# Performance work log

Hardware: AMD Instinct MI355X
Metric: run time of the kernel (lower is better)

Reference implementation:

```python
import jax, jax.numpy as jnp
import numpy as np
import math

S, HID = 2048, 2048
NH, Q_LORA, KV_LORA = 16, 1536, 512
NOPE, ROPE, VDIM = 128, 64, 128
HEAD = NOPE + ROPE  # 192
BLK = 128
EPS = 1e-6
MSCALE = 0.1 * 1.0 * math.log(40.0) + 1.0
SOFTMAX_SCALE = HEAD ** -0.5 * MSCALE * MSCALE


def _dequant(w, s, blk=BLK):
    # w: [out,in] stored quantized values, s: [ceil(out/blk), ceil(in/blk)] block scale_inv
    so = jnp.repeat(s, blk, axis=0)[: w.shape[0]]
    se = jnp.repeat(so, blk, axis=1)[:, : w.shape[1]]
    return w * se


def _mm_dq(x, w, s):
    # mm_w8a16_dq_forward: x @ dequant(w).T
    return x @ _dequant(w, s).T


def _rmsnorm(x, w, eps=EPS):
    var = jnp.mean(x * x, axis=-1, keepdims=True)
    return x * jax.lax.rsqrt(var + eps) * w


def _rotate_half(x):
    h = x.shape[-1] // 2
    return jnp.concatenate([-x[..., h:], x[..., :h]], axis=-1)


def setup_inputs() -> dict:
    key = jax.random.key(0)
    ks = jax.random.split(key, 16)
    d = {
        'hidden_states': jax.random.normal(ks[0], (S, HID), jnp.float32),
        'wq_a': jax.random.normal(ks[1], (Q_LORA, HID), jnp.float32),
        'sq_a': jax.random.uniform(ks[2], (12, 16), jnp.float32) * 0.02 + 0.005,
        'wq_b': jax.random.normal(ks[3], (NH * HEAD, Q_LORA), jnp.float32),
        'sq_b': jax.random.uniform(ks[4], (24, 12), jnp.float32) * 0.02 + 0.005,
        'wkv_a': jax.random.normal(ks[5], (KV_LORA + ROPE, HID), jnp.float32),
        'skv_a': jax.random.uniform(ks[6], (5, 16), jnp.float32) * 0.02 + 0.005,
        'wkv_b': jax.random.normal(ks[7], (NH * (NOPE + VDIM), KV_LORA), jnp.float32),
        'skv_b': jax.random.uniform(ks[8], (32, 4), jnp.float32) * 0.02 + 0.005,
        'wo': jax.random.normal(ks[9], (HID, NH * VDIM), jnp.float32),
        'so': jax.random.uniform(ks[10], (16, 16), jnp.float32) * 0.02 + 0.005,
        'q_ln_w': jnp.ones((Q_LORA,), jnp.float32),
        'kv_ln_w': jnp.ones((KV_LORA,), jnp.float32),
    }
    pos = jnp.arange(S, dtype=jnp.float32)[:, None]
    inv = 1.0 / (10000.0 ** (jnp.arange(0, ROPE, 2, dtype=jnp.float32) / ROPE))
    ang = pos * inv[None, :]
    ang = jnp.concatenate([ang, ang], axis=-1)  # [S, 64]
    d['cos'] = jnp.cos(ang)
    d['sin'] = jnp.sin(ang)
    return d


def reference(hidden_states, cos, sin, wq_a, sq_a, wq_b, sq_b, wkv_a, skv_a,
              wkv_b, skv_b, wo, so, q_ln_w, kv_ln_w):
    # Q low-rank path: q_a -> rmsnorm -> q_b
    lq = _mm_dq(hidden_states, wq_a, sq_a)                 # [S, q_lora]
    q = _mm_dq(_rmsnorm(lq, q_ln_w), wq_b, sq_b)           # [S, NH*HEAD]
    q = q.reshape(S, NH, HEAD)
    q_nope, q_pe = q[..., :NOPE], q[..., NOPE:]            # [S,NH,128], [S,NH,64]

    # KV low-rank + MQA rope path
    lkv = _mm_dq(hidden_states, wkv_a, skv_a)              # [S, kv_lora+rope]
    kv_nope = _rmsnorm(lkv[:, :KV_LORA], kv_ln_w)          # [S, kv_lora]
    k_pe = lkv[:, KV_LORA:]                                # [S, 64] (shared across heads)
    kvb = _mm_dq(kv_nope, wkv_b, skv_b).reshape(S, NH, NOPE + VDIM)
    k_nope, v = kvb[..., :NOPE], kvb[..., NOPE:]           # [S,NH,128] each

    # RoPE (rotate-half) on the pe parts
    q_pe = q_pe * cos[:, None, :] + _rotate_half(q_pe) * sin[:, None, :]
    k_pe = k_pe * cos + _rotate_half(k_pe) * sin           # [S, 64]

    # prefill MLA attention with causal mask
    scores = (jnp.einsum('shd,thd->hst', q_nope, k_nope)
              + jnp.einsum('shd,td->hst', q_pe, k_pe)) * SOFTMAX_SCALE
    causal = jnp.tril(jnp.ones((S, S), bool))
    scores = jnp.where(causal[None], scores, -jnp.inf)
    probs = jax.nn.softmax(scores, axis=-1)                # [NH,S,S]
    attn = jnp.einsum('hst,thd->shd', probs, v).reshape(S, NH * VDIM)

    return _mm_dq(attn, wo, so)                            # [S, HID]
```

## Files before the change

### kernel.cpp

```cpp
#include <hip/hip_runtime.h>

typedef unsigned short u16;
typedef unsigned int u32;
typedef __attribute__((ext_vector_type(8))) short bf16x8;
typedef __attribute__((ext_vector_type(4))) float f32x4;
typedef __attribute__((ext_vector_type(16))) float f32x16;
typedef __attribute__((ext_vector_type(4))) unsigned short u16x4;

#define S_LEN 2048
#define HIDDEN 2048
#define NHEAD 16
#define QLORA 1536
#define KVLORA 512
#define NOPE_D 128
#define ROPE_D 64
#define V_D 128
#define HEAD_D 192
#define NCOMB 2176
#define LOG2E 1.442695041f

__device__ __constant__ float SM_SCALE_C = (float)(0.07216878364870323 *
    ((0.1 * 3.6888794541139363 + 1.0) * (0.1 * 3.6888794541139363 + 1.0)));

__device__ inline u16 f2bf(float f) {
    union { float f; unsigned int u; } v; v.f = f;
    unsigned int r = v.u + 0x7FFFu + ((v.u >> 16) & 1u);
    return (u16)(r >> 16);
}
__device__ inline float bf2f(u16 b) {
    union { unsigned int u; float f; } v; v.u = ((unsigned int)b) << 16;
    return v.f;
}
__device__ inline void gload_lds16(const u16* g, u16* l) {
    __builtin_amdgcn_global_load_lds(
        (const __attribute__((address_space(1))) void*)g,
        (__attribute__((address_space(3))) void*)l, 16, 0, 0);
}
__device__ __forceinline__ void dequant_row8(const float* __restrict__ W, const float* __restrict__ Sc,
                                             u16* __restrict__ out, int n, int K, int sc_cols, int k) {
    float sc = Sc ? Sc[(n >> 7) * sc_cols + (k >> 7)] : 1.0f;
    f32x4 v0 = *(const f32x4*)(W + (size_t)n * K + k);
    f32x4 v1 = *(const f32x4*)(W + (size_t)n * K + k + 4);
    bf16x8 o;
    #pragma unroll
    for (int i = 0; i < 4; ++i) {
        o[i]     = (short)f2bf(v0[i] * sc);
        o[i + 4] = (short)f2bf(v1[i] * sc);
    }
    *(bf16x8*)(out + (size_t)n * K + k) = o;
}

__device__ __forceinline__ int xcd_swizzle(int orig, int nwg) {
    int qq = nwg >> 3, rr = nwg & 7, xcd = orig & 7, loc = orig >> 3;
    return (xcd < rr) ? (xcd * (qq + 1) + loc)
                      : (rr * (qq + 1) + (xcd - rr) * qq + loc);
}

__device__ __forceinline__ void gemm_core(
    const u16* __restrict__ A, const u16* __restrict__ W, u16* __restrict__ C,
    int M, int N, int Ktot, int Ksub, int bm, int bn, int bz,
    u16* As, u16* Ws) {
    const int tid = threadIdx.x;
    const int lane = tid & 63;
    const int wv = tid >> 6;
    const int wm = wv >> 1, wn = wv & 1;
    const int lr = lane & 15, lk = lane >> 4;
    const int srow = lane >> 3;
    const int schunk = lane & 7;

    f32x4 acc[4][4] = {};

    const int kbeg = bz * Ksub;
    const int kend = kbeg + Ksub;
    for (int k0 = kbeg; k0 < kend; k0 += 64) {
        __syncthreads();
        #pragma unroll
        for (int i = 0; i < 4; ++i) {
            int t = (wv * 4 + i) * 8 + srow;
            int cs = (schunk ^ (t & 7)) << 3;
            gload_lds16(A + (size_t)(bm + t) * Ktot + k0 + cs, &As[(wv * 4 + i) * 512]);
            gload_lds16(W + (size_t)(bn + t) * Ktot + k0 + cs, &Ws[(wv * 4 + i) * 512]);
        }
        __syncthreads();
        #pragma unroll
        for (int kh = 0; kh < 2; ++kh) {
            bf16x8 af[4], bfr[4];
            #pragma unroll
            for (int mi = 0; mi < 4; ++mi) {
                int r = wm * 64 + mi * 16 + lr;
                af[mi] = *(const bf16x8*)&As[r * 64 + (((kh * 4 + lk) ^ (lr & 7)) << 3)];
            }
            #pragma unroll
            for (int ni = 0; ni < 4; ++ni) {
                int r = wn * 64 + ni * 16 + lr;
                bfr[ni] = *(const bf16x8*)&Ws[r * 64 + (((kh * 4 + lk) ^ (lr & 7)) << 3)];
            }
            #pragma unroll
            for (int mi = 0; mi < 4; ++mi)
                #pragma unroll
                for (int ni = 0; ni < 4; ++ni)
                    acc[mi][ni] = __builtin_amdgcn_mfma_f32_16x16x32_bf16(af[mi], bfr[ni], acc[mi][ni], 0, 0, 0);
        }
    }

    u16* Pb = C + (size_t)bz * M * N;
    #pragma unroll
    for (int mi = 0; mi < 4; ++mi)
        #pragma unroll
        for (int ni = 0; ni < 4; ++ni)
            #pragma unroll
            for (int j = 0; j < 4; ++j) {
                int r = bm + wm * 64 + mi * 16 + lk * 4 + j;
                int c = bn + wn * 64 + ni * 16 + lr;
                if (c < N) Pb[(size_t)r * N + c] = f2bf(acc[mi][ni][j]);
            }
}

__global__ __launch_bounds__(256)
void prep_weights_a(const float* __restrict__ hs,
                    const float* __restrict__ wq_a, const float* __restrict__ sq_a,
                    const float* __restrict__ wkv_a, const float* __restrict__ skv_a,
                    u16* __restrict__ hs_bf, u16* __restrict__ wcomb) {
    int r = blockIdx.x * 4 + (threadIdx.x >> 6);
    const float* W; const float* Sc; u16* out; int n, sc_cols;
    if (r < 2048)      { W = hs;    Sc = 0;      out = hs_bf; n = r;        sc_cols = 0; }
    else if (r < 3584) { W = wq_a;  Sc = sq_a;   out = wcomb; n = r - 2048; sc_cols = 16; }
    else               { W = wkv_a; Sc = skv_a;  out = wcomb + (size_t)QLORA * 2048; n = r - 3584; sc_cols = 16; }
    for (int k = (threadIdx.x & 63) * 8; k < 2048; k += 512)
        dequant_row8(W, Sc, out, n, 2048, sc_cols, k);
}

__global__ __launch_bounds__(256)
void gemm_comb_prepw(const u16* __restrict__ hs_bf, const u16* __restrict__ wcomb,
                     u16* __restrict__ arena,
                     const float* __restrict__ wq_b, const float* __restrict__ sq_b,
                     const float* __restrict__ wkv_b, const float* __restrict__ skv_b,
                     const float* __restrict__ wo, const float* __restrict__ so,
                     u16* __restrict__ wqb_bf, u16* __restrict__ wkvb_bf,
                     u16* __restrict__ wo_bf) {
    __shared__ u16 As[128 * 64];
    __shared__ u16 Ws[128 * 64];
    const int NWG = 17 * 16 * 4 + 2304;
    const int wg = xcd_swizzle(blockIdx.x, NWG);
    if (wg < 17 * 16 * 4) {
        const int bn = (wg % 17) * 128;
        const int bm = ((wg / 17) % 16) * 128;
        const int bz = wg / (17 * 16);
        gemm_core(hs_bf, wcomb, arena, S_LEN, NCOMB, HIDDEN, HIDDEN / 4, bm, bn, bz, As, Ws);
    } else {
        const int w2 = wg - 17 * 16 * 4;
        int r = w2 * 4 + (threadIdx.x >> 6);
        const float* W; const float* Sc; u16* out; int n, K, sc_cols;
        if (r < 3072)      { W = wq_b;  Sc = sq_b;  out = wqb_bf;  n = r;        K = 1536; sc_cols = 12; }
        else if (r < 7168) { W = wkv_b; Sc = skv_b; out = wkvb_bf; n = r - 3072; K = 512;  sc_cols = 4; }
        else               { W = wo;    Sc = so;    out = wo_bf;   n = r - 7168; K = 2048; sc_cols = 16; }
        for (int k = (threadIdx.x & 63) * 8; k < K; k += 512)
            dequant_row8(W, Sc, out, n, K, sc_cols, k);
    }
}

__global__ __launch_bounds__(256)
void gemm_bf16(const u16* __restrict__ A, const u16* __restrict__ W,
               u16* __restrict__ C, int M, int N, int Ktot, int Ksub) {
    __shared__ u16 As[128 * 64];
    __shared__ u16 Ws[128 * 64];
    const int gx = gridDim.x, gy = gridDim.y;
    const int nwg = gx * gy * gridDim.z;
    const int orig = blockIdx.x + gx * (blockIdx.y + gy * blockIdx.z);
    const int wg = xcd_swizzle(orig, nwg);
    const int bn = (wg % gx) * 128;
    const int bm = ((wg / gx) % gy) * 128;
    const int bz = wg / (gx * gy);
    gemm_core(A, W, C, M, N, Ktot, Ksub, bm, bn, bz, As, Ws);
}

__global__ __launch_bounds__(256)
void gemm_qh_kvb(const u16* __restrict__ lqn, const u16* __restrict__ wqb, u16* __restrict__ arena,
                 const u16* __restrict__ kvn, const u16* __restrict__ wkvb, u16* __restrict__ kvb) {
    __shared__ u16 As[128 * 64];
    __shared__ u16 Ws[128 * 64];
    const int NWG = 24 * 16 * 3 + 32 * 16;
    const int wg = xcd_swizzle(blockIdx.x, NWG);
    if (wg < 24 * 16 * 3) {
        const int bn = (wg % 24) * 128;
        const int bm = ((wg / 24) % 16) * 128;
        const int bz = wg / (24 * 16);
        gemm_core(lqn, wqb, arena, S_LEN, NHEAD * HEAD_D, QLORA, 512, bm, bn, bz, As, Ws);
    } else {
        const int w2 = wg - 24 * 16 * 3;
        const int bn = (w2 % 32) * 128;
        const int bm = (w2 / 32) * 128;
        gemm_core(kvn, wkvb, kvb, S_LEN, NHEAD * 256, KVLORA, 512, bm, bn, 0, As, Ws);
    }
}

__global__ __launch_bounds__(256)
void reduce_rms_comb(const u16* __restrict__ P,
                     const float* __restrict__ q_ln, const float* __restrict__ kv_ln,
                     u16* __restrict__ lqn, u16* __restrict__ kvn, u16* __restrict__ kpe) {
    __shared__ float vbuf[NCOMB];
    __shared__ float r2[2][4];
    const int row = blockIdx.x;
    const u16* p0 = P + (size_t)row * NCOMB;
    const size_t st = (size_t)S_LEN * NCOMB;
    float ssq = 0.f, ssk = 0.f;
    for (int c = threadIdx.x * 8; c < NCOMB; c += 2048) {
        bf16x8 a0 = *(const bf16x8*)(p0 + c);
        bf16x8 a1 = *(const bf16x8*)(p0 + st + c);
        bf16x8 a2 = *(const bf16x8*)(p0 + 2 * st + c);
        bf16x8 a3 = *(const bf16x8*)(p0 + 3 * st + c);
        float s = 0.f;
        #pragma unroll
        for (int j = 0; j < 8; ++j) {
            float v = bf2f((u16)a0[j]) + bf2f((u16)a1[j]) + bf2f((u16)a2[j]) + bf2f((u16)a3[j]);
            vbuf[c + j] = v;
            s += v * v;
        }
        if (c < QLORA) ssq += s;
        else if (c < QLORA + KVLORA) ssk += s;
    }
    #pragma unroll
    for (int off = 1; off < 64; off <<= 1) {
        ssq += __shfl_xor(ssq, off, 64);
        ssk += __shfl_xor(ssk, off, 64);
    }
    if ((threadIdx.x & 63) == 0) {
        r2[0][threadIdx.x >> 6] = ssq;
        r2[1][threadIdx.x >> 6] = ssk;
    }
    __syncthreads();
    float rsq = rsqrtf((r2[0][0] + r2[0][1] + r2[0][2] + r2[0][3]) / (float)QLORA + 1e-6f);
    float rsk = rsqrtf((r2[1][0] + r2[1][1] + r2[1][2] + r2[1][3]) / (float)KVLORA + 1e-6f);
    for (int c = threadIdx.x * 8; c < NCOMB; c += 2048) {
        bf16x8 o;
        if (c < QLORA) {
            #pragma unroll
            for (int j = 0; j < 8; ++j) o[j] = (short)f2bf(vbuf[c + j] * rsq * q_ln[c + j]);
            *(bf16x8*)(lqn + (size_t)row * QLORA + c) = o;
        } else if (c < QLORA + KVLORA) {
            int cc = c - QLORA;
            #pragma unroll
            for (int j = 0; j < 8; ++j) o[j] = (short)f2bf(vbuf[c + j] * rsk * kv_ln[cc + j]);
            *(bf16x8*)(kvn + (size_t)row * KVLORA + cc) = o;
        } else if (c < QLORA + KVLORA + ROPE_D) {
            int cc = c - QLORA - KVLORA;
            #pragma unroll
            for (int j = 0; j < 8; ++j) o[j] = (short)f2bf(vbuf[c + j]);
            *(bf16x8*)(kpe + (size_t)row * ROPE_D + cc) = o;
        }
    }
}

__global__ __launch_bounds__(256)
void prep_qkv_frag(const u16* __restrict__ P, const u16* __restrict__ kvb,
                   const u16* __restrict__ kpe, const float* __restrict__ cosb,
                   const float* __restrict__ sinb, u16* __restrict__ qfrag,
                   u16* __restrict__ kfrag, u16* __restrict__ vfrag) {
    __shared__ u16 Vs[32][136];
    const int sblk = blockIdx.x, h = blockIdx.y;
    if (blockIdx.z == 0) {
        const float sm = SM_SCALE_C;
        const size_t st = (size_t)S_LEN * (NHEAD * HEAD_D);
        #pragma unroll
        for (int c = 0; c < 3; ++c) {
            int idx = c * 256 + threadIdx.x;
            int kk = idx >> 6;
            int lane = idx & 63;
            int s = sblk * 32 + (lane & 31);
            int d0 = kk * 16 + (lane >> 5) * 8;
            const u16* p0 = P + (size_t)s * (NHEAD * HEAD_D) + h * HEAD_D;
            float x[8];
            {
                bf16x8 a0 = *(const bf16x8*)(p0 + d0);
                bf16x8 a1 = *(const bf16x8*)(p0 + st + d0);
                bf16x8 a2 = *(const bf16x8*)(p0 + 2 * st + d0);
                #pragma unroll
                for (int j = 0; j < 8; ++j)
                    x[j] = bf2f((u16)a0[j]) + bf2f((u16)a1[j]) + bf2f((u16)a2[j]);
            }
            bf16x8 o;
            if (d0 < NOPE_D) {
                #pragma unroll
                for (int j = 0; j < 8; ++j) o[j] = (short)f2bf(x[j] * sm);
            } else {
                int r0 = d0 - NOPE_D;
                int rp = (r0 + 32) & 63;
                float rv[8];
                bf16x8 b0 = *(const bf16x8*)(p0 + NOPE_D + rp);
                bf16x8 b1 = *(const bf16x8*)(p0 + st + NOPE_D + rp);
                bf16x8 b2 = *(const bf16x8*)(p0 + 2 * st + NOPE_D + rp);
                #pragma unroll
                for (int j = 0; j < 8; ++j)
                    rv[j] = bf2f((u16)b0[j]) + bf2f((u16)b1[j]) + bf2f((u16)b2[j]);
                float sign = (r0 < 32) ? -1.f : 1.f;
                #pragma unroll
                for (int j = 0; j < 8; ++j) {
                    float cs = cosb[s * ROPE_D + r0 + j];
                    float sn = sinb[s * ROPE_D + r0 + j];
                    o[j] = (short)f2bf((x[j] * cs + sign * rv[j] * sn) * sm);
                }
            }
            *(bf16x8*)(qfrag + (((size_t)h * 64 + sblk) * 12 + kk) * 512 + lane * 8) = o;
        }
    } else {
        #pragma unroll
        for (int it = 0; it < 2; ++it) {
            int idx = it * 256 + threadIdx.x;
            int r = idx >> 4;
            int c8 = (idx & 15) * 8;
            int s = sblk * 32 + r;
            *(bf16x8*)&Vs[r][c8] = *(const bf16x8*)(kvb + (size_t)s * (NHEAD * 256) + h * 256 + NOPE_D + c8);
        }
        #pragma unroll
        for (int c = 0; c < 3; ++c) {
            int idx = c * 256 + threadIdx.x;
            int kk = idx >> 6;
            int lane = idx & 63;
            int s = sblk * 32 + (lane & 31);
            int d0 = kk * 16 + (lane >> 5) * 8;
            bf16x8 o;
            if (d0 < NOPE_D) {
                o = *(const bf16x8*)(kvb + (size_t)s * (NHEAD * 256) + h * 256 + d0);
            } else {
                int r0 = d0 - NOPE_D;
                const u16* kp = kpe + (size_t)s * ROPE_D;
                bf16x8 x = *(const bf16x8*)(kp + r0);
                bf16x8 rv = *(const bf16x8*)(kp + ((r0 + 32) & 63));
                float sign = (r0 < 32) ? -1.f : 1.f;
                #pragma unroll
                for (int j = 0; j < 8; ++j) {
                    float cs = cosb[s * ROPE_D + r0 + j];
                    float sn = sinb[s * ROPE_D + r0 + j];
                    o[j] = (short)f2bf(bf2f((u16)x[j]) * cs + sign * bf2f((u16)rv[j]) * sn);
                }
            }
            *(bf16x8*)(kfrag + (((size_t)h * 64 + sblk) * 12 + kk) * 512 + lane * 8) = o;
        }
        __syncthreads();
        #pragma unroll
        for (int it = 0; it < 2; ++it) {
            int idx = it * 256 + threadIdx.x;
            int fi = idx >> 6;
            int lane = idx & 63;
            int bb = fi >> 1, h16 = fi & 1;
            int col = bb * 32 + (lane & 31);
            int row0 = h16 * 16 + (lane >> 5) * 8;
            bf16x8 o;
            #pragma unroll
            for (int j = 0; j < 8; ++j) o[j] = (short)Vs[row0 + j][col];
            *(bf16x8*)(vfrag + (((size_t)h * 64 + sblk) * 8 + fi) * 512 + lane * 8) = o;
        }
    }
}

__global__ void reduce_out(const u16* __restrict__ P, float* __restrict__ out, int n) {
    int i = (blockIdx.x * blockDim.x + threadIdx.x) * 8;
    if (i >= n) return;
    bf16x8 a0 = *(const bf16x8*)(P + i);
    bf16x8 a1 = *(const bf16x8*)(P + (size_t)n + i);
    bf16x8 a2 = *(const bf16x8*)(P + 2 * (size_t)n + i);
    bf16x8 a3 = *(const bf16x8*)(P + 3 * (size_t)n + i);
    f32x4 o0, o1;
    #pragma unroll
    for (int j = 0; j < 4; ++j) {
        o0[j] = bf2f((u16)a0[j]) + bf2f((u16)a1[j]) + bf2f((u16)a2[j]) + bf2f((u16)a3[j]);
        o1[j] = bf2f((u16)a0[j + 4]) + bf2f((u16)a1[j + 4]) + bf2f((u16)a2[j + 4]) + bf2f((u16)a3[j + 4]);
    }
    *(f32x4*)(out + i) = o0;
    *(f32x4*)(out + i + 4) = o1;
}

__global__ __launch_bounds__(256, 2)
void flash_attn4(const u16* __restrict__ qfrag, const u16* __restrict__ kfrag,
                 const u16* __restrict__ vfrag, u16* __restrict__ attn) {
    __shared__ float OB[3][128][32];
    __shared__ float MB[3][2][32];

    const int tid = threadIdx.x, lane = tid & 63, wq = tid >> 6;
    const int b = blockIdx.x;
    const int t = 63 - (b >> 4);
    const int h = ((b & 7) << 1) | ((b >> 3) & 1);
    const int q0 = t * 32;
    const int lq = lane & 31;
    const int hi = lane >> 5;

    const int n = t + 1;
    const int s_lo = (wq * n) >> 2;
    const int s_hi = ((wq + 1) * n) >> 2;

    bf16x8 qfr[12];
    {
        const u16* qb = qfrag + (((size_t)h * 64 + t) * 12) * 512 + lane * 8;
        #pragma unroll
        for (int kk = 0; kk < 12; ++kk) qfr[kk] = *(const bf16x8*)(qb + kk * 512);
    }

    const u16* kfb = kfrag + ((size_t)h * 64 * 12) * 512 + lane * 8;
    const u16* vfb = vfrag + ((size_t)h * 64 * 8) * 512 + lane * 8;

    f32x16 oa[4] = {};
    float mrun = -3.0e38f, lrun = 0.f;

    bf16x8 kcur[12];
    {
        int psub = (s_lo < s_hi) ? s_lo : 0;
        const u16* kp = kfb + (size_t)psub * 12 * 512;
        #pragma unroll
        for (int kk = 0; kk < 12; ++kk)
            kcur[kk] = *(const bf16x8*)(kp + kk * 512);
    }

    for (int sub = s_lo; sub < s_hi; ++sub) {
        f32x16 s0 = {}, s1 = {};
        __builtin_amdgcn_s_setprio(1);
        #pragma unroll
        for (int kk = 0; kk < 12; kk += 2) {
            s0 = __builtin_amdgcn_mfma_f32_32x32x16_bf16(kcur[kk], qfr[kk], s0, 0, 0, 0);
            s1 = __builtin_amdgcn_mfma_f32_32x32x16_bf16(kcur[kk + 1], qfr[kk + 1], s1, 0, 0, 0);
        }
        __builtin_amdgcn_s_setprio(0);
        {
            int nsub = (sub + 1 < s_hi) ? sub + 1 : sub;
            const u16* kp = kfb + (size_t)nsub * 12 * 512;
            #pragma unroll
            for (int kk = 0; kk < 12; ++kk)
                kcur[kk] = *(const bf16x8*)(kp + kk * 512);
        }
        bf16x8 va[8];
        {
            const u16* vp = vfb + (size_t)sub * 8 * 512;
            #pragma unroll
            for (int fi = 0; fi < 8; ++fi)
                va[fi] = *(const bf16x8*)(vp + fi * 512);
        }
        f32x16 sv = s0 + s1;
        if (sub == t) {
            #pragma unroll
            for (int r = 0; r < 16; ++r) {
                int krow = (r & 3) + 8 * (r >> 2) + 4 * hi;
                if (krow > lq) sv[r] = -3.0e38f;
            }
        }
        float tm = sv[0];
        #pragma unroll
        for (int r = 1; r < 16; ++r) tm = fmaxf(tm, sv[r]);
        tm = fmaxf(tm, __shfl_xor(tm, 32, 64));
        if (!__all(tm - mrun <= 8.f)) {
            float mn = fmaxf(mrun, tm);
            float scl = exp2f((mrun - mn) * LOG2E);
            mrun = mn;
            lrun *= scl;
            #pragma unroll
            for (int bb = 0; bb < 4; ++bb)
                #pragma unroll
                for (int r = 0; r < 16; ++r) oa[bb][r] *= scl;
        }
        float p[16];
        float psum = 0.f;
        #pragma unroll
        for (int r = 0; r < 16; ++r) {
            p[r] = exp2f((sv[r] - mrun) * LOG2E);
            psum += p[r];
        }
        psum += __shfl_xor(psum, 32, 64);
        lrun += psum;
        u32 pw[8], sw[8];
        #pragma unroll
        for (int i = 0; i < 8; ++i)
            pw[i] = (u32)f2bf(p[2 * i]) | ((u32)f2bf(p[2 * i + 1]) << 16);
        #pragma unroll
        for (int i = 0; i < 8; ++i)
            sw[i] = (u32)__shfl_xor((int)pw[i], 32, 64);
        union { u32 w[4]; bf16x8 v; } bf0, bf1;
        bf0.w[0] = hi ? sw[2] : pw[0];
        bf0.w[1] = hi ? sw[3] : pw[1];
        bf0.w[2] = hi ? pw[2] : sw[0];
        bf0.w[3] = hi ? pw[3] : sw[1];
        bf1.w[0] = hi ? sw[6] : pw[4];
        bf1.w[1] = hi ? sw[7] : pw[5];
        bf1.w[2] = hi ? pw[6] : sw[4];
        bf1.w[3] = hi ? pw[7] : sw[5];
        __builtin_amdgcn_s_setprio(1);
        #pragma unroll
        for (int bb = 0; bb < 4; ++bb) {
            oa[bb] = __builtin_amdgcn_mfma_f32_32x32x16_bf16(va[bb * 2],     bf0.v, oa[bb], 0, 0, 0);
            oa[bb] = __builtin_amdgcn_mfma_f32_32x32x16_bf16(va[bb * 2 + 1], bf1.v, oa[bb], 0, 0, 0);
        }
        __builtin_amdgcn_s_setprio(0);
    }

    if (wq) {
        #pragma unroll
        for (int bb = 0; bb < 4; ++bb)
            #pragma unroll
            for (int r = 0; r < 16; ++r) {
                int dv = bb * 32 + (r & 3) + 8 * (r >> 2) + 4 * hi;
                OB[wq - 1][dv][lq] = oa[bb][r];
            }
        if (lane < 32) {
            MB[wq - 1][0][lane] = mrun;
            MB[wq - 1][1][lane] = lrun;
        }
    }
    __syncthreads();
    if (!wq) {
        float m1 = MB[0][0][lq], l1 = MB[0][1][lq];
        float m2 = MB[1][0][lq], l2 = MB[1][1][lq];
        float m3 = MB[2][0][lq], l3 = MB[2][1][lq];
        float M = fmaxf(fmaxf(mrun, m1), fmaxf(m2, m3));
        float e0 = exp2f((mrun - M) * LOG2E);
        float e1 = exp2f((m1 - M) * LOG2E);
        float e2 = exp2f((m2 - M) * LOG2E);
        float e3 = exp2f((m3 - M) * LOG2E);
        float L = lrun * e0 + l1 * e1 + l2 * e2 + l3 * e3;
        float inv = 1.0f / L;
        u16* ob = attn + (size_t)(q0 + lq) * (NHEAD * V_D) + h * V_D;
        #pragma unroll
        for (int bb = 0; bb < 4; ++bb)
            #pragma unroll
            for (int rq = 0; rq < 4; ++rq) {
                u16x4 pk;
                #pragma unroll
                for (int rb = 0; rb < 4; ++rb) {
                    int r = rq * 4 + rb;
                    int dv = bb * 32 + rb + 8 * rq + 4 * hi;
                    float o = (oa[bb][r] * e0 + OB[0][dv][lq] * e1 +
                               OB[1][dv][lq] * e2 + OB[2][dv][lq] * e3) * inv;
                    pk[rb] = f2bf(o);
                }
                *(u16x4*)(ob + bb * 32 + 8 * rq + 4 * hi) = pk;
            }
    }
}

extern "C" void kernel_launch(void* const* d_in, const int* in_sizes, int n_in,
                              void* d_out, int out_size, void* d_ws, size_t ws_size,
                              hipStream_t stream) {
    const float* hs    = (const float*)d_in[0];
    const float* wq_a  = (const float*)d_in[1];
    const float* sq_a  = (const float*)d_in[2];
    const float* wq_b  = (const float*)d_in[3];
    const float* sq_b  = (const float*)d_in[4];
    const float* wkv_a = (const float*)d_in[5];
    const float* skv_a = (const float*)d_in[6];
    const float* wkv_b = (const float*)d_in[7];
    const float* skv_b = (const float*)d_in[8];
    const float* wo    = (const float*)d_in[9];
    const float* so    = (const float*)d_in[10];
    const float* q_ln  = (const float*)d_in[11];
    const float* kv_ln = (const float*)d_in[12];
    const float* cosb  = (const float*)d_in[13];
    const float* sinb  = (const float*)d_in[14];
    float* out = (float*)d_out;

    char* ws = (char*)d_ws;
    size_t off = 0;
    auto alloc = [&](size_t bytes) -> void* {
        void* p = ws + off; off += (bytes + 255) & ~(size_t)255; return p;
    };
    u16* hs_bf  = (u16*)alloc((size_t)S_LEN * HIDDEN * 2);
    u16* lqn    = (u16*)alloc((size_t)S_LEN * QLORA * 2);
    u16* kvn    = (u16*)alloc((size_t)S_LEN * KVLORA * 2);
    u16* kpe    = (u16*)alloc((size_t)S_LEN * ROPE_D * 2);
    u16* kvb    = (u16*)alloc((size_t)S_LEN * NHEAD * 256 * 2);
    u16* attn   = (u16*)alloc((size_t)S_LEN * NHEAD * V_D * 2);
    u16* qfrag  = (u16*)alloc((size_t)NHEAD * 64 * 12 * 512 * 2);
    u16* kfrag  = (u16*)alloc((size_t)NHEAD * 64 * 12 * 512 * 2);
    u16* vfrag  = (u16*)alloc((size_t)NHEAD * 64 * 8 * 512 * 2);
    u16* wcomb  = (u16*)alloc((size_t)NCOMB * HIDDEN * 2);
    u16* wqb_bf  = (u16*)alloc((size_t)(NHEAD * HEAD_D) * QLORA * 2);
    u16* wkvb_bf = (u16*)alloc((size_t)(NHEAD * 256) * KVLORA * 2);
    u16* wo_bf   = (u16*)alloc((size_t)HIDDEN * (NHEAD * V_D) * 2);
    u16* arena  = (u16*)alloc((size_t)4 * S_LEN * NCOMB * 2);

    prep_weights_a<<<1040, 256, 0, stream>>>(hs, wq_a, sq_a, wkv_a, skv_a, hs_bf, wcomb);

    gemm_comb_prepw<<<3392, 256, 0, stream>>>(hs_bf, wcomb, arena,
        wq_b, sq_b, wkv_b, skv_b, wo, so, wqb_bf, wkvb_bf, wo_bf);
    reduce_rms_comb<<<S_LEN, 256, 0, stream>>>(arena, q_ln, kv_ln, lqn, kvn, kpe);

    gemm_qh_kvb<<<24 * 16 * 3 + 32 * 16, 256, 0, stream>>>(lqn, wqb_bf, arena, kvn, wkvb_bf, kvb);

    prep_qkv_frag<<<dim3(64, NHEAD, 2), 256, 0, stream>>>(arena, kvb, kpe, cosb, sinb,
        qfrag, kfrag, vfrag);

    flash_attn4<<<1024, 256, 0, stream>>>(qfrag, kfrag, vfrag, attn);

    gemm_bf16<<<dim3(16, 16, 4), 256, 0, stream>>>(attn, wo_bf, arena,
        S_LEN, HIDDEN, NHEAD * V_D, (NHEAD * V_D) / 4);
    reduce_out<<<S_LEN * HIDDEN / 8 / 256, 256, 0, stream>>>(arena, out, S_LEN * HIDDEN);
}
```

Measured before the change: 224.1 us.

## Double-buffer GEMM LDS tiles and unfuse weight prep from first GEMM

The shared GEMM core now double-buffers its A and W shared-memory tiles. It issues the next K-slice's global-to-LDS loads before running MFMAs on the current slice, and raises wave priority around the MFMA block. This hides load latency and drops one barrier per iteration, but doubles LDS per workgroup (64KB), which may lower occupancy. All weight dequantisation now happens in a single prep kernel ahead of a plain split-K GEMM, replacing the old GEMM kernel that interleaved dequant blocks. The arena is also resized.

```diff
diff --git a/kernel.cpp b/kernel.cpp
--- a/kernel.cpp
+++ b/kernel.cpp
@@ -36,19 +36,6 @@
         (const __attribute__((address_space(1))) void*)g,
         (__attribute__((address_space(3))) void*)l, 16, 0, 0);
 }
-__device__ __forceinline__ void dequant_row8(const float* __restrict__ W, const float* __restrict__ Sc,
-                                             u16* __restrict__ out, int n, int K, int sc_cols, int k) {
-    float sc = Sc ? Sc[(n >> 7) * sc_cols + (k >> 7)] : 1.0f;
-    f32x4 v0 = *(const f32x4*)(W + (size_t)n * K + k);
-    f32x4 v1 = *(const f32x4*)(W + (size_t)n * K + k + 4);
-    bf16x8 o;
-    #pragma unroll
-    for (int i = 0; i < 4; ++i) {
-        o[i]     = (short)f2bf(v0[i] * sc);
-        o[i + 4] = (short)f2bf(v1[i] * sc);
-    }
-    *(bf16x8*)(out + (size_t)n * K + k) = o;
-}
 
 __device__ __forceinline__ int xcd_swizzle(int orig, int nwg) {
     int qq = nwg >> 3, rr = nwg & 7, xcd = orig & 7, loc = orig >> 3;
@@ -56,10 +43,42 @@
                       : (rr * (qq + 1) + (xcd - rr) * qq + loc);
 }
 
+__global__ __launch_bounds__(256)
+void prep_weights(const float* __restrict__ hs,
+                  const float* __restrict__ wq_a, const float* __restrict__ sq_a,
+                  const float* __restrict__ wq_b, const float* __restrict__ sq_b,
+                  const float* __restrict__ wkv_a, const float* __restrict__ skv_a,
+                  const float* __restrict__ wkv_b, const float* __restrict__ skv_b,
+                  const float* __restrict__ wo, const float* __restrict__ so,
+                  u16* __restrict__ hs_bf, u16* __restrict__ wcomb,
+                  u16* __restrict__ wqb_bf, u16* __restrict__ wkvb_bf,
+                  u16* __restrict__ wo_bf) {
+    int r = blockIdx.x * 4 + (threadIdx.x >> 6);
+    const float* W; const float* Sc; u16* out; int n, K, sc_cols;
+    if (r < 2048)       { W = hs;    Sc = 0;      out = hs_bf;   n = r;        K = 2048; sc_cols = 0; }
+    else if (r < 3584)  { W = wq_a;  Sc = sq_a;   out = wcomb;   n = r - 2048; K = 2048; sc_cols = 16; }
+    else if (r < 4160)  { W = wkv_a; Sc = skv_a;  out = wcomb + (size_t)QLORA * 2048; n = r - 3584; K = 2048; sc_cols = 16; }
+    else if (r < 7232)  { W = wq_b;  Sc = sq_b;   out = wqb_bf;  n = r - 4160; K = 1536; sc_cols = 12; }
+    else if (r < 11328) { W = wkv_b; Sc = skv_b;  out = wkvb_bf; n = r - 7232; K = 512;  sc_cols = 4; }
+    else                { W = wo;    Sc = so;     out = wo_bf;   n = r - 11328; K = 2048; sc_cols = 16; }
+    for (int k = (threadIdx.x & 63) * 8; k < K; k += 512) {
+        float sc = Sc ? Sc[(n >> 7) * sc_cols + (k >> 7)] : 1.0f;
+        f32x4 v0 = *(const f32x4*)(W + (size_t)n * K + k);
+        f32x4 v1 = *(const f32x4*)(W + (size_t)n * K + k + 4);
+        bf16x8 o;
+        #pragma unroll
+        for (int i = 0; i < 4; ++i) {
+            o[i]     = (short)f2bf(v0[i] * sc);
+            o[i + 4] = (short)f2bf(v1[i] * sc);
+        }
+        *(bf16x8*)(out + (size_t)n * K + k) = o;
+    }
+}
+
 __device__ __forceinline__ void gemm_core(
     const u16* __restrict__ A, const u16* __restrict__ W, u16* __restrict__ C,
     int M, int N, int Ktot, int Ksub, int bm, int bn, int bz,
-    u16* As, u16* Ws) {
+    u16 (*As)[128 * 64], u16 (*Ws)[128 * 64]) {
     const int tid = threadIdx.x;
     const int lane = tid & 63;
     const int wv = tid >> 6;
@@ -71,36 +90,46 @@
     f32x4 acc[4][4] = {};
 
     const int kbeg = bz * Ksub;
-    const int kend = kbeg + Ksub;
-    for (int k0 = kbeg; k0 < kend; k0 += 64) {
-        __syncthreads();
+    const int nst = Ksub >> 6;
+
+    auto stage = [&](int buf, int k0) {
         #pragma unroll
         for (int i = 0; i < 4; ++i) {
             int t = (wv * 4 + i) * 8 + srow;
             int cs = (schunk ^ (t & 7)) << 3;
-            gload_lds16(A + (size_t)(bm + t) * Ktot + k0 + cs, &As[(wv * 4 + i) * 512]);
-            gload_lds16(W + (size_t)(bn + t) * Ktot + k0 + cs, &Ws[(wv * 4 + i) * 512]);
-        }
-        __syncthreads();
+            gload_lds16(A + (size_t)(bm + t) * Ktot + k0 + cs, &As[buf][(wv * 4 + i) * 512]);
+            gload_lds16(W + (size_t)(bn + t) * Ktot + k0 + cs, &Ws[buf][(wv * 4 + i) * 512]);
+        }
+    };
+
+    stage(0, kbeg);
+    __syncthreads();
+    int cur = 0;
+    for (int t = 0; t < nst; ++t) {
+        if (t + 1 < nst) stage(cur ^ 1, kbeg + (t + 1) * 64);
         #pragma unroll
         for (int kh = 0; kh < 2; ++kh) {
             bf16x8 af[4], bfr[4];
             #pragma unroll
             for (int mi = 0; mi < 4; ++mi) {
                 int r = wm * 64 + mi * 16 + lr;
-                af[mi] = *(const bf16x8*)&As[r * 64 + (((kh * 4 + lk) ^ (lr & 7)) << 3)];
+                af[mi] = *(const bf16x8*)&As[cur][r * 64 + (((kh * 4 + lk) ^ (lr & 7)) << 3)];
             }
             #pragma unroll
             for (int ni = 0; ni < 4; ++ni) {
                 int r = wn * 64 + ni * 16 + lr;
-                bfr[ni] = *(const bf16x8*)&Ws[r * 64 + (((kh * 4 + lk) ^ (lr & 7)) << 3)];
-            }
+                bfr[ni] = *(const bf16x8*)&Ws[cur][r * 64 + (((kh * 4 + lk) ^ (lr & 7)) << 3)];
+            }
+            __builtin_amdgcn_s_setprio(1);
             #pragma unroll
             for (int mi = 0; mi < 4; ++mi)
                 #pragma unroll
                 for (int ni = 0; ni < 4; ++ni)
                     acc[mi][ni] = __builtin_amdgcn_mfma_f32_16x16x32_bf16(af[mi], bfr[ni], acc[mi][ni], 0, 0, 0);
-        }
+            __builtin_amdgcn_s_setprio(0);
+        }
+        __syncthreads();
+        cur ^= 1;
     }
 
     u16* Pb = C + (size_t)bz * M * N;
@@ -117,53 +146,10 @@
 }
 
 __global__ __launch_bounds__(256)
-void prep_weights_a(const float* __restrict__ hs,
-                    const float* __restrict__ wq_a, const float* __restrict__ sq_a,
-                    const float* __restrict__ wkv_a, const float* __restrict__ skv_a,
-                    u16* __restrict__ hs_bf, u16* __restrict__ wcomb) {
-    int r = blockIdx.x * 4 + (threadIdx.x >> 6);
-    const float* W; const float* Sc; u16* out; int n, sc_cols;
-    if (r < 2048)      { W = hs;    Sc = 0;      out = hs_bf; n = r;        sc_cols = 0; }
-    else if (r < 3584) { W = wq_a;  Sc = sq_a;   out = wcomb; n = r - 2048; sc_cols = 16; }
-    else               { W = wkv_a; Sc = skv_a;  out = wcomb + (size_t)QLORA * 2048; n = r - 3584; sc_cols = 16; }
-    for (int k = (threadIdx.x & 63) * 8; k < 2048; k += 512)
-        dequant_row8(W, Sc, out, n, 2048, sc_cols, k);
-}
-
-__global__ __launch_bounds__(256)
-void gemm_comb_prepw(const u16* __restrict__ hs_bf, const u16* __restrict__ wcomb,
-                     u16* __restrict__ arena,
-                     const float* __restrict__ wq_b, const float* __restrict__ sq_b,
-                     const float* __restrict__ wkv_b, const float* __restrict__ skv_b,
-                     const float* __restrict__ wo, const float* __restrict__ so,
-                     u16* __restrict__ wqb_bf, u16* __restrict__ wkvb_bf,
-                     u16* __restrict__ wo_bf) {
-    __shared__ u16 As[128 * 64];
-    __shared__ u16 Ws[128 * 64];
-    const int NWG = 17 * 16 * 4 + 2304;
-    const int wg = xcd_swizzle(blockIdx.x, NWG);
-    if (wg < 17 * 16 * 4) {
-        const int bn = (wg % 17) * 128;
-        const int bm = ((wg / 17) % 16) * 128;
-        const int bz = wg / (17 * 16);
-        gemm_core(hs_bf, wcomb, arena, S_LEN, NCOMB, HIDDEN, HIDDEN / 4, bm, bn, bz, As, Ws);
-    } else {
-        const int w2 = wg - 17 * 16 * 4;
-        int r = w2 * 4 + (threadIdx.x >> 6);
-        const float* W; const float* Sc; u16* out; int n, K, sc_cols;
-        if (r < 3072)      { W = wq_b;  Sc = sq_b;  out = wqb_bf;  n = r;        K = 1536; sc_cols = 12; }
-        else if (r < 7168) { W = wkv_b; Sc = skv_b; out = wkvb_bf; n = r - 3072; K = 512;  sc_cols = 4; }
-        else               { W = wo;    Sc = so;    out = wo_bf;   n = r - 7168; K = 2048; sc_cols = 16; }
-        for (int k = (threadIdx.x & 63) * 8; k < K; k += 512)
-            dequant_row8(W, Sc, out, n, K, sc_cols, k);
-    }
-}
-
-__global__ __launch_bounds__(256)
 void gemm_bf16(const u16* __restrict__ A, const u16* __restrict__ W,
                u16* __restrict__ C, int M, int N, int Ktot, int Ksub) {
-    __shared__ u16 As[128 * 64];
-    __shared__ u16 Ws[128 * 64];
+    __shared__ u16 As[2][128 * 64];
+    __shared__ u16 Ws[2][128 * 64];
     const int gx = gridDim.x, gy = gridDim.y;
     const int nwg = gx * gy * gridDim.z;
     const int orig = blockIdx.x + gx * (blockIdx.y + gy * blockIdx.z);
@@ -177,8 +163,8 @@
 __global__ __launch_bounds__(256)
 void gemm_qh_kvb(const u16* __restrict__ lqn, const u16* __restrict__ wqb, u16* __restrict__ arena,
                  const u16* __restrict__ kvn, const u16* __restrict__ wkvb, u16* __restrict__ kvb) {
-    __shared__ u16 As[128 * 64];
-    __shared__ u16 Ws[128 * 64];
+    __shared__ u16 As[2][128 * 64];
+    __shared__ u16 Ws[2][128 * 64];
     const int NWG = 24 * 16 * 3 + 32 * 16;
     const int wg = xcd_swizzle(blockIdx.x, NWG);
     if (wg < 24 * 16 * 3) {
@@ -571,12 +557,14 @@
     u16* wqb_bf  = (u16*)alloc((size_t)(NHEAD * HEAD_D) * QLORA * 2);
     u16* wkvb_bf = (u16*)alloc((size_t)(NHEAD * 256) * KVLORA * 2);
     u16* wo_bf   = (u16*)alloc((size_t)HIDDEN * (NHEAD * V_D) * 2);
-    u16* arena  = (u16*)alloc((size_t)4 * S_LEN * NCOMB * 2);
-
-    prep_weights_a<<<1040, 256, 0, stream>>>(hs, wq_a, sq_a, wkv_a, skv_a, hs_bf, wcomb);
-
-    gemm_comb_prepw<<<3392, 256, 0, stream>>>(hs_bf, wcomb, arena,
-        wq_b, sq_b, wkv_b, skv_b, wo, so, wqb_bf, wkvb_bf, wo_bf);
+    u16* arena  = (u16*)alloc((size_t)3 * S_LEN * (NHEAD * HEAD_D) * 2);
+
+    prep_weights<<<3344, 256, 0, stream>>>(
+        hs, wq_a, sq_a, wq_b, sq_b, wkv_a, skv_a, wkv_b, skv_b, wo, so,
+        hs_bf, wcomb, wqb_bf, wkvb_bf, wo_bf);
+
+    gemm_bf16<<<dim3(NCOMB / 128, S_LEN / 128, 4), 256, 0, stream>>>(hs_bf, wcomb, arena,
+        S_LEN, NCOMB, HIDDEN, HIDDEN / 4);
     reduce_rms_comb<<<S_LEN, 256, 0, stream>>>(arena, q_ln, kv_ln, lqn, kvn, kpe);
 
     gemm_qh_kvb<<<24 * 16 * 3 + 32 * 16, 256, 0, stream>>>(lqn, wqb_bf, arena, kvn, wkvb_bf, kvb);
```

Measured after the change: 199.0 us. 11.2% less time.
